# Kernel optimization log

Hardware: AMD Instinct MI355X
Metric: run time of the kernel (lower is better)

Reference implementation:

```python
import jax, jax.numpy as jnp
import numpy as np

INPUTDIM = 512
OUTDIM = 512
GRIDSIZE = 50


def setup_inputs() -> dict:
    key = jax.random.key(0)
    k1, k2 = jax.random.split(key)
    x = jax.random.normal(k1, (8, 256, INPUTDIM), dtype=jnp.float32)
    scale = 1.0 / (np.sqrt(INPUTDIM) * np.sqrt(GRIDSIZE))
    fouriercoeffs = jax.random.normal(k2, (2 * GRIDSIZE, INPUTDIM, OUTDIM), dtype=jnp.float32) * scale
    bias = jnp.zeros((OUTDIM,), dtype=jnp.float32)
    return {"x": x, "fouriercoeffs": fouriercoeffs, "bias": bias}


def reference(x, fouriercoeffs, bias):
    # x: (B, W, I); fouriercoeffs: (2G, I, O); bias: (O,)
    B, W, I = x.shape
    G = fouriercoeffs.shape[0] // 2
    k = jnp.arange(1, G + 1, dtype=x.dtype)  # (G,)
    angles = x[..., None] * k * jnp.pi  # (B, W, I, G)
    # features: (B, W, I, 2G) with [sin | cos] order matching torch.cat
    features = jnp.concatenate([jnp.sin(angles), jnp.cos(angles)], axis=-1)
    features = features.reshape(B * W, I, 2 * G)
    y = jnp.einsum("bik,kio->bo", features, fouriercoeffs)  # (B*W, O)
    y = y.reshape(B, W, -1) + bias
    return y
```

## Files before the change

### kernel.cpp

```cpp
#include <hip/hip_runtime.h>
#include <hip/hip_bf16.h>

#define NS 100
#define TILE_BYTES 8192

typedef float f32x4 __attribute__((ext_vector_type(4)));
typedef float f32x2 __attribute__((ext_vector_type(2)));
typedef short s16x8 __attribute__((ext_vector_type(8)));
typedef unsigned int u32x4 __attribute__((ext_vector_type(4)));

static __device__ __forceinline__ unsigned int cvtpk(float a, float b) {
  unsigned int r;
  asm("v_cvt_pk_bf16_f32 %0, %1, %2" : "=v"(r) : "v"(a), "v"(b));
  return r;
}

__global__ void fkan_zero(float* __restrict__ out) {
  int idx = blockIdx.x * 256 + threadIdx.x;
  f32x4 z = {0.f, 0.f, 0.f, 0.f};
  *(f32x4*)(out + (size_t)idx * 4) = z;
}

__global__ void fkan_prep(const float* __restrict__ C, unsigned short* __restrict__ Bt) {
  __shared__ float ldsF[32][136];
  const int bx = blockIdx.x;
  const int s = bx % NS;
  const int spnt = bx / NS;
  const int sp = spnt & 15, nt = spnt >> 4;
  const int f = (s >> 1) + 50 * (s & 1);
  const int t = threadIdx.x;

  const float* src = C + ((size_t)f * 512 + sp * 32) * 512 + nt * 128;
  const int col4 = t & 31, row0 = t >> 5;
  #pragma unroll
  for (int rep = 0; rep < 4; ++rep) {
    int r = row0 + rep * 8;
    f32x4 v = *(const f32x4*)(src + (size_t)r * 512 + col4 * 4);
    *(f32x4*)&ldsF[r][col4 * 4] = v;
  }
  __syncthreads();

  char* dst = (char*)Bt + (size_t)(spnt * NS + s) * TILE_BYTES;
  #pragma unroll
  for (int q = 0; q < 2; ++q) {
    const int h = t + q * 256;
    const int o = h >> 2;
    const int ca = h & 3;
    const int cd = ca ^ ((o >> 1) & 3);
    u32x4 p;
    p[0] = cvtpk(ldsF[cd*8+0][o], ldsF[cd*8+1][o]);
    p[1] = cvtpk(ldsF[cd*8+2][o], ldsF[cd*8+3][o]);
    p[2] = cvtpk(ldsF[cd*8+4][o], ldsF[cd*8+5][o]);
    p[3] = cvtpk(ldsF[cd*8+6][o], ldsF[cd*8+7][o]);
    *(u32x4*)(dst + h * 16) = p;
  }
}

__global__ __launch_bounds__(256, 2) void fkan_gemm(
    const float* __restrict__ x, const unsigned short* __restrict__ Bt,
    const float* __restrict__ bias, float* __restrict__ out) {
  __shared__ __attribute__((aligned(16))) char Bs[4][TILE_BYTES];

  const int tid  = threadIdx.x;
  const int lane = tid & 63;
  const int wid  = tid >> 6;
  const int wm   = wid >> 1, wn = wid & 1;
  const int d    = blockIdx.x;
  const int bid  = (d & 7) * 128 + (d >> 3);
  const int mt   = bid & 15;
  const int nt   = (bid >> 4) & 3;
  const int sp   = bid >> 6;
  const int m0 = mt * 128, n0 = nt * 128;
  const int lrow = lane & 15, lkg = lane >> 4;
  const int swz  = (lrow >> 1) & 3;

  f32x2 sk[4][4], ck[4][4], s1[4][4], c1[4][4];
  #pragma unroll
  for (int mi = 0; mi < 4; ++mi) {
    const float* xp = x + (size_t)(m0 + wm*64 + mi*16 + lrow) * 512 + sp*32 + lkg*8;
    f32x4 xa = *(const f32x4*)xp;
    f32x4 xb = *(const f32x4*)(xp + 4);
    #pragma unroll
    for (int p = 0; p < 4; ++p) {
      #pragma unroll
      for (int e = 0; e < 2; ++e) {
        int j = p * 2 + e;
        float xv = (j < 4) ? xa[j] : xb[j - 4];
        float r = xv * 0.5f;
        asm("v_fract_f32 %0, %1" : "=v"(r) : "v"(r));
        float sv, cv;
        asm("v_sin_f32 %0, %1" : "=v"(sv) : "v"(r));
        asm("v_cos_f32 %0, %1" : "=v"(cv) : "v"(r));
        s1[mi][p][e] = sv; c1[mi][p][e] = cv;
        sk[mi][p][e] = sv; ck[mi][p][e] = cv;
      }
    }
  }

  f32x4 acc[4][4];
  #pragma unroll
  for (int mi = 0; mi < 4; ++mi)
    #pragma unroll
    for (int ni = 0; ni < 4; ++ni)
      acc[mi][ni] = (f32x4){0.f, 0.f, 0.f, 0.f};

  const char* gsrc = (const char*)Bt + (size_t)(nt * 16 + sp) * NS * TILE_BYTES + tid * 16;

  auto stage = [&](int buf, int s) {
    const char* p = gsrc + (size_t)s * TILE_BYTES;
    __builtin_amdgcn_global_load_lds(
        (const __attribute__((address_space(1))) unsigned int*)(p),
        (__attribute__((address_space(3))) unsigned int*)(&Bs[buf][tid * 16]), 16, 0, 0);
    __builtin_amdgcn_global_load_lds(
        (const __attribute__((address_space(1))) unsigned int*)(p + 4096),
        (__attribute__((address_space(3))) unsigned int*)(&Bs[buf][4096 + tid * 16]), 16, 0, 0);
  };

  auto iter = [&](int s, f32x2 (&st)[4][4]) {
    s16x8 af[4];
    #pragma unroll
    for (int mi = 0; mi < 4; ++mi) {
      u32x4 pk;
      pk[0] = cvtpk(st[mi][0][0], st[mi][0][1]);
      pk[1] = cvtpk(st[mi][1][0], st[mi][1][1]);
      pk[2] = cvtpk(st[mi][2][0], st[mi][2][1]);
      pk[3] = cvtpk(st[mi][3][0], st[mi][3][1]);
      af[mi] = __builtin_bit_cast(s16x8, pk);
    }
    if (s < NS - 2) asm volatile("s_waitcnt vmcnt(2)" ::: "memory");
    else            asm volatile("s_waitcnt vmcnt(0)" ::: "memory");
    __builtin_amdgcn_s_barrier();
    if (s < NS - 2) stage((s + 2) & 3, s + 2);
    const char* base = &Bs[s & 3][0];
    s16x8 bfr[4];
    #pragma unroll
    for (int ni = 0; ni < 4; ++ni) {
      int o_loc = wn * 64 + ni * 16 + lrow;
      bfr[ni] = *(const s16x8*)(base + o_loc * 64 + ((lkg ^ swz) << 4));
    }
    __builtin_amdgcn_s_setprio(1);
    #pragma unroll
    for (int mi = 0; mi < 4; ++mi)
      #pragma unroll
      for (int ni = 0; ni < 4; ++ni)
        acc[mi][ni] = __builtin_amdgcn_mfma_f32_16x16x32_bf16(af[mi], bfr[ni], acc[mi][ni], 0, 0, 0);
    __builtin_amdgcn_s_setprio(0);
  };

  stage(0, 0);
  stage(1, 1);
  #pragma unroll 1
  for (int kh = 0; kh < 50; ++kh) {
    iter(2 * kh, sk);
    iter(2 * kh + 1, ck);
    #pragma unroll
    for (int mi = 0; mi < 4; ++mi)
      #pragma unroll
      for (int p = 0; p < 4; ++p) {
        f32x2 so = sk[mi][p], co = ck[mi][p];
        sk[mi][p] = so * c1[mi][p] + co * s1[mi][p];
        ck[mi][p] = co * c1[mi][p] - so * s1[mi][p];
      }
  }

  #pragma unroll
  for (int ni = 0; ni < 4; ++ni) {
    const int col = n0 + wn * 64 + ni * 16 + lrow;
    const float bv = (sp == 0) ? bias[col] : 0.0f;
    #pragma unroll
    for (int mi = 0; mi < 4; ++mi) {
      const int row = m0 + wm * 64 + mi * 16 + lkg * 4;
      #pragma unroll
      for (int j = 0; j < 4; ++j)
        atomicAdd(out + (size_t)(row + j) * 512 + col, acc[mi][ni][j] + bv);
    }
  }
}

extern "C" void kernel_launch(void* const* d_in, const int* in_sizes, int n_in,
                              void* d_out, int out_size, void* d_ws, size_t ws_size,
                              hipStream_t stream) {
  const float* x    = (const float*)d_in[0];
  const float* C    = (const float*)d_in[1];
  const float* bias = (const float*)d_in[2];
  float* out = (float*)d_out;
  unsigned short* Bt = (unsigned short*)d_ws;

  fkan_zero<<<dim3(1024), dim3(256), 0, stream>>>(out);
  fkan_prep<<<dim3(6400), dim3(256), 0, stream>>>(C, Bt);
  fkan_gemm<<<dim3(1024), dim3(256), 0, stream>>>(x, Bt, bias, out);
}
```

Baseline: 314.6 us.

## Fold zeroing into prep, remap warps to 32x128, deepen LDS pipeline

```diff
diff --git a/kernel.cpp b/kernel.cpp
--- a/kernel.cpp
+++ b/kernel.cpp
@@ -15,13 +15,8 @@
   return r;
 }
 
-__global__ void fkan_zero(float* __restrict__ out) {
-  int idx = blockIdx.x * 256 + threadIdx.x;
-  f32x4 z = {0.f, 0.f, 0.f, 0.f};
-  *(f32x4*)(out + (size_t)idx * 4) = z;
-}
-
-__global__ void fkan_prep(const float* __restrict__ C, unsigned short* __restrict__ Bt) {
+__global__ void fkan_prep(const float* __restrict__ C, unsigned short* __restrict__ Bt,
+                          float* __restrict__ out) {
   __shared__ float ldsF[32][136];
   const int bx = blockIdx.x;
   const int s = bx % NS;
@@ -30,13 +25,17 @@
   const int f = (s >> 1) + 50 * (s & 1);
   const int t = threadIdx.x;
 
+  if (bx < 1024) {
+    f32x4 z = {0.f, 0.f, 0.f, 0.f};
+    *(f32x4*)(out + (size_t)bx * 1024 + t * 4) = z;
+  }
+
   const float* src = C + ((size_t)f * 512 + sp * 32) * 512 + nt * 128;
   const int col4 = t & 31, row0 = t >> 5;
   #pragma unroll
   for (int rep = 0; rep < 4; ++rep) {
     int r = row0 + rep * 8;
-    f32x4 v = *(const f32x4*)(src + (size_t)r * 512 + col4 * 4);
-    *(f32x4*)&ldsF[r][col4 * 4] = v;
+    *(f32x4*)&ldsF[r][col4 * 4] = *(const f32x4*)(src + (size_t)r * 512 + col4 * 4);
   }
   __syncthreads();
 
@@ -44,27 +43,24 @@
   #pragma unroll
   for (int q = 0; q < 2; ++q) {
     const int h = t + q * 256;
-    const int o = h >> 2;
-    const int ca = h & 3;
-    const int cd = ca ^ ((o >> 1) & 3);
+    const int c = h >> 7, o = h & 127;
     u32x4 p;
-    p[0] = cvtpk(ldsF[cd*8+0][o], ldsF[cd*8+1][o]);
-    p[1] = cvtpk(ldsF[cd*8+2][o], ldsF[cd*8+3][o]);
-    p[2] = cvtpk(ldsF[cd*8+4][o], ldsF[cd*8+5][o]);
-    p[3] = cvtpk(ldsF[cd*8+6][o], ldsF[cd*8+7][o]);
+    p[0] = cvtpk(ldsF[c*8+0][o], ldsF[c*8+1][o]);
+    p[1] = cvtpk(ldsF[c*8+2][o], ldsF[c*8+3][o]);
+    p[2] = cvtpk(ldsF[c*8+4][o], ldsF[c*8+5][o]);
+    p[3] = cvtpk(ldsF[c*8+6][o], ldsF[c*8+7][o]);
     *(u32x4*)(dst + h * 16) = p;
   }
 }
 
-__global__ __launch_bounds__(256, 2) void fkan_gemm(
+__global__ __launch_bounds__(256, 3) void fkan_gemm(
     const float* __restrict__ x, const unsigned short* __restrict__ Bt,
     const float* __restrict__ bias, float* __restrict__ out) {
-  __shared__ __attribute__((aligned(16))) char Bs[4][TILE_BYTES];
+  __shared__ __attribute__((aligned(16))) char Bs[6][TILE_BYTES];
 
   const int tid  = threadIdx.x;
   const int lane = tid & 63;
   const int wid  = tid >> 6;
-  const int wm   = wid >> 1, wn = wid & 1;
   const int d    = blockIdx.x;
   const int bid  = (d & 7) * 128 + (d >> 3);
   const int mt   = bid & 15;
@@ -72,12 +68,11 @@
   const int sp   = bid >> 6;
   const int m0 = mt * 128, n0 = nt * 128;
   const int lrow = lane & 15, lkg = lane >> 4;
-  const int swz  = (lrow >> 1) & 3;
 
-  f32x2 sk[4][4], ck[4][4], s1[4][4], c1[4][4];
+  f32x2 sk[2][4], ck[2][4], s1[2][4], c1[2][4];
   #pragma unroll
-  for (int mi = 0; mi < 4; ++mi) {
-    const float* xp = x + (size_t)(m0 + wm*64 + mi*16 + lrow) * 512 + sp*32 + lkg*8;
+  for (int mi = 0; mi < 2; ++mi) {
+    const float* xp = x + (size_t)(m0 + wid*32 + mi*16 + lrow) * 512 + sp*32 + lkg*8;
     f32x4 xa = *(const f32x4*)xp;
     f32x4 xb = *(const f32x4*)(xp + 4);
     #pragma unroll
@@ -97,29 +92,36 @@
     }
   }
 
-  f32x4 acc[4][4];
+  f32x4 acc[2][8];
   #pragma unroll
-  for (int mi = 0; mi < 4; ++mi)
+  for (int mi = 0; mi < 2; ++mi)
     #pragma unroll
-    for (int ni = 0; ni < 4; ++ni)
+    for (int ni = 0; ni < 8; ++ni)
       acc[mi][ni] = (f32x4){0.f, 0.f, 0.f, 0.f};
 
-  const char* gsrc = (const char*)Bt + (size_t)(nt * 16 + sp) * NS * TILE_BYTES + tid * 16;
+  const char* gp = (const char*)Bt + (size_t)(nt * 16 + sp) * NS * TILE_BYTES + tid * 16;
+  int cur = 0;
 
-  auto stage = [&](int buf, int s) {
-    const char* p = gsrc + (size_t)s * TILE_BYTES;
+  auto stage = [&](int buf) {
     __builtin_amdgcn_global_load_lds(
-        (const __attribute__((address_space(1))) unsigned int*)(p),
+        (const __attribute__((address_space(1))) unsigned int*)(gp),
         (__attribute__((address_space(3))) unsigned int*)(&Bs[buf][tid * 16]), 16, 0, 0);
     __builtin_amdgcn_global_load_lds(
-        (const __attribute__((address_space(1))) unsigned int*)(p + 4096),
+        (const __attribute__((address_space(1))) unsigned int*)(gp + 4096),
         (__attribute__((address_space(3))) unsigned int*)(&Bs[buf][4096 + tid * 16]), 16, 0, 0);
+    gp += TILE_BYTES;
   };
 
-  auto iter = [&](int s, f32x2 (&st)[4][4]) {
-    s16x8 af[4];
+  auto iter = [&](f32x2 (&st)[2][4], bool do_stage, int wait_sel) {
+    if (wait_sel == 2)      asm volatile("s_waitcnt vmcnt(4)" ::: "memory");
+    else if (wait_sel == 1) asm volatile("s_waitcnt vmcnt(2)" ::: "memory");
+    else                    asm volatile("s_waitcnt vmcnt(0)" ::: "memory");
+    __builtin_amdgcn_s_barrier();
+    if (do_stage) { int b = cur + 3; if (b >= 6) b -= 6; stage(b); }
+
+    s16x8 af[2];
     #pragma unroll
-    for (int mi = 0; mi < 4; ++mi) {
+    for (int mi = 0; mi < 2; ++mi) {
       u32x4 pk;
       pk[0] = cvtpk(st[mi][0][0], st[mi][0][1]);
       pk[1] = cvtpk(st[mi][1][0], st[mi][1][1]);
@@ -127,49 +129,55 @@
       pk[3] = cvtpk(st[mi][3][0], st[mi][3][1]);
       af[mi] = __builtin_bit_cast(s16x8, pk);
     }
-    if (s < NS - 2) asm volatile("s_waitcnt vmcnt(2)" ::: "memory");
-    else            asm volatile("s_waitcnt vmcnt(0)" ::: "memory");
-    __builtin_amdgcn_s_barrier();
-    if (s < NS - 2) stage((s + 2) & 3, s + 2);
-    const char* base = &Bs[s & 3][0];
-    s16x8 bfr[4];
+    const char* base = &Bs[cur][0] + lkg * 2048 + lrow * 16;
     #pragma unroll
-    for (int ni = 0; ni < 4; ++ni) {
-      int o_loc = wn * 64 + ni * 16 + lrow;
-      bfr[ni] = *(const s16x8*)(base + o_loc * 64 + ((lkg ^ swz) << 4));
+    for (int h = 0; h < 2; ++h) {
+      s16x8 bfr[4];
+      #pragma unroll
+      for (int q = 0; q < 4; ++q)
+        bfr[q] = *(const s16x8*)(base + (h * 4 + q) * 256);
+      __builtin_amdgcn_s_setprio(1);
+      #pragma unroll
+      for (int mi = 0; mi < 2; ++mi)
+        #pragma unroll
+        for (int q = 0; q < 4; ++q)
+          acc[mi][h*4+q] = __builtin_amdgcn_mfma_f32_16x16x32_bf16(af[mi], bfr[q], acc[mi][h*4+q], 0, 0, 0);
+      __builtin_amdgcn_s_setprio(0);
     }
-    __builtin_amdgcn_s_setprio(1);
-    #pragma unroll
-    for (int mi = 0; mi < 4; ++mi)
-      #pragma unroll
-      for (int ni = 0; ni < 4; ++ni)
-        acc[mi][ni] = __builtin_amdgcn_mfma_f32_16x16x32_bf16(af[mi], bfr[ni], acc[mi][ni], 0, 0, 0);
-    __builtin_amdgcn_s_setprio(0);
+    cur = (cur + 1 == 6) ? 0 : cur + 1;
   };
 
-  stage(0, 0);
-  stage(1, 1);
-  #pragma unroll 1
-  for (int kh = 0; kh < 50; ++kh) {
-    iter(2 * kh, sk);
-    iter(2 * kh + 1, ck);
+  auto recur = [&]() {
     #pragma unroll
-    for (int mi = 0; mi < 4; ++mi)
+    for (int mi = 0; mi < 2; ++mi)
       #pragma unroll
       for (int p = 0; p < 4; ++p) {
         f32x2 so = sk[mi][p], co = ck[mi][p];
         sk[mi][p] = so * c1[mi][p] + co * s1[mi][p];
         ck[mi][p] = co * c1[mi][p] - so * s1[mi][p];
       }
+  };
+
+  stage(0); stage(1); stage(2);
+  #pragma unroll 1
+  for (int kh = 0; kh < 48; ++kh) {
+    iter(sk, true, 2);
+    iter(ck, true, 2);
+    recur();
   }
+  iter(sk, true, 2);
+  iter(ck, false, 2);
+  recur();
+  iter(sk, false, 1);
+  iter(ck, false, 0);
 
   #pragma unroll
-  for (int ni = 0; ni < 4; ++ni) {
-    const int col = n0 + wn * 64 + ni * 16 + lrow;
+  for (int ni = 0; ni < 8; ++ni) {
+    const int col = n0 + ni * 16 + lrow;
     const float bv = (sp == 0) ? bias[col] : 0.0f;
     #pragma unroll
-    for (int mi = 0; mi < 4; ++mi) {
-      const int row = m0 + wm * 64 + mi * 16 + lkg * 4;
+    for (int mi = 0; mi < 2; ++mi) {
+      const int row = m0 + wid * 32 + mi * 16 + lkg * 4;
       #pragma unroll
       for (int j = 0; j < 4; ++j)
         atomicAdd(out + (size_t)(row + j) * 512 + col, acc[mi][ni][j] + bv);
@@ -186,7 +194,6 @@
   float* out = (float*)d_out;
   unsigned short* Bt = (unsigned short*)d_ws;
 
-  fkan_zero<<<dim3(1024), dim3(256), 0, stream>>>(out);
-  fkan_prep<<<dim3(6400), dim3(256), 0, stream>>>(C, Bt);
+  fkan_prep<<<dim3(6400), dim3(256), 0, stream>>>(C, Bt, out);
   fkan_gemm<<<dim3(1024), dim3(256), 0, stream>>>(x, Bt, bias, out);
 }
```

Measured after the change: 281.7 us. 1.12x faster.

## Use single-wave 64x64 GEMM blocks, barrier-free pipeline, fuse zeroing into prep

Applied to the files above, without the earlier changes.

```diff
diff --git a/kernel.cpp b/kernel.cpp
--- a/kernel.cpp
+++ b/kernel.cpp
@@ -2,7 +2,7 @@
 #include <hip/hip_bf16.h>
 
 #define NS 100
-#define TILE_BYTES 8192
+#define TILE_BYTES 4096
 
 typedef float f32x4 __attribute__((ext_vector_type(4)));
 typedef float f32x2 __attribute__((ext_vector_type(2)));
@@ -15,69 +15,52 @@
   return r;
 }
 
-__global__ void fkan_zero(float* __restrict__ out) {
-  int idx = blockIdx.x * 256 + threadIdx.x;
-  f32x4 z = {0.f, 0.f, 0.f, 0.f};
-  *(f32x4*)(out + (size_t)idx * 4) = z;
-}
-
-__global__ void fkan_prep(const float* __restrict__ C, unsigned short* __restrict__ Bt) {
-  __shared__ float ldsF[32][136];
+__global__ void fkan_prep(const float* __restrict__ C, unsigned short* __restrict__ Bt,
+                          float* __restrict__ out) {
   const int bx = blockIdx.x;
   const int s = bx % NS;
-  const int spnt = bx / NS;
-  const int sp = spnt & 15, nt = spnt >> 4;
+  const int q = bx / NS;
+  const int sp = q & 15, nt = q >> 4;
   const int f = (s >> 1) + 50 * (s & 1);
   const int t = threadIdx.x;
 
-  const float* src = C + ((size_t)f * 512 + sp * 32) * 512 + nt * 128;
-  const int col4 = t & 31, row0 = t >> 5;
+  if (bx < 1024) {
+    f32x4 z = {0.f, 0.f, 0.f, 0.f};
+    *(f32x4*)(out + (size_t)bx * 1024 + t * 4) = z;
+  }
+
+  const int c = t >> 6, col = t & 63;
+  const float* src = C + ((size_t)f * 512 + sp * 32 + c * 8) * 512 + nt * 64 + col;
+  float v[8];
   #pragma unroll
-  for (int rep = 0; rep < 4; ++rep) {
-    int r = row0 + rep * 8;
-    f32x4 v = *(const f32x4*)(src + (size_t)r * 512 + col4 * 4);
-    *(f32x4*)&ldsF[r][col4 * 4] = v;
-  }
-  __syncthreads();
-
-  char* dst = (char*)Bt + (size_t)(spnt * NS + s) * TILE_BYTES;
-  #pragma unroll
-  for (int q = 0; q < 2; ++q) {
-    const int h = t + q * 256;
-    const int o = h >> 2;
-    const int ca = h & 3;
-    const int cd = ca ^ ((o >> 1) & 3);
-    u32x4 p;
-    p[0] = cvtpk(ldsF[cd*8+0][o], ldsF[cd*8+1][o]);
-    p[1] = cvtpk(ldsF[cd*8+2][o], ldsF[cd*8+3][o]);
-    p[2] = cvtpk(ldsF[cd*8+4][o], ldsF[cd*8+5][o]);
-    p[3] = cvtpk(ldsF[cd*8+6][o], ldsF[cd*8+7][o]);
-    *(u32x4*)(dst + h * 16) = p;
-  }
+  for (int j = 0; j < 8; ++j) v[j] = src[(size_t)j * 512];
+  u32x4 p;
+  p[0] = cvtpk(v[0], v[1]);
+  p[1] = cvtpk(v[2], v[3]);
+  p[2] = cvtpk(v[4], v[5]);
+  p[3] = cvtpk(v[6], v[7]);
+  *(u32x4*)((char*)Bt + (size_t)bx * TILE_BYTES + t * 16) = p;
 }
 
-__global__ __launch_bounds__(256, 2) void fkan_gemm(
+__global__ __launch_bounds__(64, 2) void fkan_gemm(
     const float* __restrict__ x, const unsigned short* __restrict__ Bt,
     const float* __restrict__ bias, float* __restrict__ out) {
   __shared__ __attribute__((aligned(16))) char Bs[4][TILE_BYTES];
 
-  const int tid  = threadIdx.x;
-  const int lane = tid & 63;
-  const int wid  = tid >> 6;
-  const int wm   = wid >> 1, wn = wid & 1;
+  const int lane = threadIdx.x;
   const int d    = blockIdx.x;
-  const int bid  = (d & 7) * 128 + (d >> 3);
-  const int mt   = bid & 15;
-  const int nt   = (bid >> 4) & 3;
-  const int sp   = bid >> 6;
-  const int m0 = mt * 128, n0 = nt * 128;
+  const int xcd  = d & 7;
+  const int u    = d >> 3;
+  const int g    = xcd * 16 + (u >> 5);
+  const int mt   = u & 31;
+  const int nt   = g >> 4, sp = g & 15;
+  const int m0 = mt * 64, n0 = nt * 64;
   const int lrow = lane & 15, lkg = lane >> 4;
-  const int swz  = (lrow >> 1) & 3;
 
   f32x2 sk[4][4], ck[4][4], s1[4][4], c1[4][4];
   #pragma unroll
   for (int mi = 0; mi < 4; ++mi) {
-    const float* xp = x + (size_t)(m0 + wm*64 + mi*16 + lrow) * 512 + sp*32 + lkg*8;
+    const float* xp = x + (size_t)(m0 + mi * 16 + lrow) * 512 + sp * 32 + lkg * 8;
     f32x4 xa = *(const f32x4*)xp;
     f32x4 xb = *(const f32x4*)(xp + 4);
     #pragma unroll
@@ -104,20 +87,29 @@
     for (int ni = 0; ni < 4; ++ni)
       acc[mi][ni] = (f32x4){0.f, 0.f, 0.f, 0.f};
 
-  const char* gsrc = (const char*)Bt + (size_t)(nt * 16 + sp) * NS * TILE_BYTES + tid * 16;
+  const char* gp = (const char*)Bt + (size_t)(nt * 16 + sp) * NS * TILE_BYTES + lane * 16;
 
-  auto stage = [&](int buf, int s) {
-    const char* p = gsrc + (size_t)s * TILE_BYTES;
-    __builtin_amdgcn_global_load_lds(
-        (const __attribute__((address_space(1))) unsigned int*)(p),
-        (__attribute__((address_space(3))) unsigned int*)(&Bs[buf][tid * 16]), 16, 0, 0);
-    __builtin_amdgcn_global_load_lds(
-        (const __attribute__((address_space(1))) unsigned int*)(p + 4096),
-        (__attribute__((address_space(3))) unsigned int*)(&Bs[buf][4096 + tid * 16]), 16, 0, 0);
+  auto stage = [&](int s) {
+    const char* p = gp + (size_t)s * TILE_BYTES;
+    #pragma unroll
+    for (int h = 0; h < 4; ++h)
+      __builtin_amdgcn_global_load_lds(
+          (const __attribute__((address_space(1))) unsigned int*)(p + h * 1024),
+          (__attribute__((address_space(3))) unsigned int*)(&Bs[s & 3][h * 1024 + lane * 16]),
+          16, 0, 0);
   };
 
-  auto iter = [&](int s, f32x2 (&st)[4][4]) {
-    s16x8 af[4];
+  auto iter = [&](int s, f32x2 (&st)[4][4], int wait_sel, bool do_stage) {
+    if (wait_sel == 2)      asm volatile("s_waitcnt vmcnt(8)" ::: "memory");
+    else if (wait_sel == 1) asm volatile("s_waitcnt vmcnt(4)" ::: "memory");
+    else                    asm volatile("s_waitcnt vmcnt(0)" ::: "memory");
+    if (do_stage) stage(s + 3);
+    const char* base = &Bs[s & 3][0] + lkg * 1024 + lrow * 16;
+    s16x8 bfr[4];
+    #pragma unroll
+    for (int ni = 0; ni < 4; ++ni)
+      bfr[ni] = *(const s16x8*)(base + ni * 256);
+    __builtin_amdgcn_s_setprio(1);
     #pragma unroll
     for (int mi = 0; mi < 4; ++mi) {
       u32x4 pk;
@@ -125,34 +117,15 @@
       pk[1] = cvtpk(st[mi][1][0], st[mi][1][1]);
       pk[2] = cvtpk(st[mi][2][0], st[mi][2][1]);
       pk[3] = cvtpk(st[mi][3][0], st[mi][3][1]);
-      af[mi] = __builtin_bit_cast(s16x8, pk);
-    }
-    if (s < NS - 2) asm volatile("s_waitcnt vmcnt(2)" ::: "memory");
-    else            asm volatile("s_waitcnt vmcnt(0)" ::: "memory");
-    __builtin_amdgcn_s_barrier();
-    if (s < NS - 2) stage((s + 2) & 3, s + 2);
-    const char* base = &Bs[s & 3][0];
-    s16x8 bfr[4];
-    #pragma unroll
-    for (int ni = 0; ni < 4; ++ni) {
-      int o_loc = wn * 64 + ni * 16 + lrow;
-      bfr[ni] = *(const s16x8*)(base + o_loc * 64 + ((lkg ^ swz) << 4));
-    }
-    __builtin_amdgcn_s_setprio(1);
-    #pragma unroll
-    for (int mi = 0; mi < 4; ++mi)
+      s16x8 af = __builtin_bit_cast(s16x8, pk);
       #pragma unroll
       for (int ni = 0; ni < 4; ++ni)
-        acc[mi][ni] = __builtin_amdgcn_mfma_f32_16x16x32_bf16(af[mi], bfr[ni], acc[mi][ni], 0, 0, 0);
+        acc[mi][ni] = __builtin_amdgcn_mfma_f32_16x16x32_bf16(af, bfr[ni], acc[mi][ni], 0, 0, 0);
+    }
     __builtin_amdgcn_s_setprio(0);
   };
 
-  stage(0, 0);
-  stage(1, 1);
-  #pragma unroll 1
-  for (int kh = 0; kh < 50; ++kh) {
-    iter(2 * kh, sk);
-    iter(2 * kh + 1, ck);
+  auto recur = [&]() {
     #pragma unroll
     for (int mi = 0; mi < 4; ++mi)
       #pragma unroll
@@ -161,15 +134,25 @@
         sk[mi][p] = so * c1[mi][p] + co * s1[mi][p];
         ck[mi][p] = co * c1[mi][p] - so * s1[mi][p];
       }
+  };
+
+  stage(0); stage(1); stage(2);
+  #pragma unroll 1
+  for (int kh = 0; kh < 49; ++kh) {
+    iter(2 * kh,     sk, 2, true);
+    iter(2 * kh + 1, ck, 2, (2 * kh + 1) <= 96);
+    recur();
   }
+  iter(98, sk, 1, false);
+  iter(99, ck, 0, false);
 
   #pragma unroll
   for (int ni = 0; ni < 4; ++ni) {
-    const int col = n0 + wn * 64 + ni * 16 + lrow;
+    const int col = n0 + ni * 16 + lrow;
     const float bv = (sp == 0) ? bias[col] : 0.0f;
     #pragma unroll
     for (int mi = 0; mi < 4; ++mi) {
-      const int row = m0 + wm * 64 + mi * 16 + lkg * 4;
+      const int row = m0 + mi * 16 + lkg * 4;
       #pragma unroll
       for (int j = 0; j < 4; ++j)
         atomicAdd(out + (size_t)(row + j) * 512 + col, acc[mi][ni][j] + bv);
@@ -186,7 +169,6 @@
   float* out = (float*)d_out;
   unsigned short* Bt = (unsigned short*)d_ws;
 
-  fkan_zero<<<dim3(1024), dim3(256), 0, stream>>>(out);
-  fkan_prep<<<dim3(6400), dim3(256), 0, stream>>>(C, Bt);
-  fkan_gemm<<<dim3(1024), dim3(256), 0, stream>>>(x, Bt, bias, out);
+  fkan_prep<<<dim3(12800), dim3(256), 0, stream>>>(C, Bt, out);
+  fkan_gemm<<<dim3(4096), dim3(64), 0, stream>>>(x, Bt, bias, out);
 }
```

New measurement: 313.3 us. Within noise of the previous version (-0.4%).
